# Performance work log

Measured on AMD Instinct MI355X. Metric: run time of the kernel, lower is better.

Reference implementation:

```python
import jax, jax.numpy as jnp
import numpy as np

T, B, C = 2048, 8, 1024
HEAD_SIZE = 128
HEAD_OUT = 128


def setup_inputs() -> dict:
    key = jax.random.key(0)
    kq, kk, kv, kwq, kwk, kwv = jax.random.split(key, 6)
    q = jax.random.normal(kq, (T, B, C), dtype=jnp.float32)
    k = jax.random.normal(kk, (T, B, C), dtype=jnp.float32)
    v = jax.random.normal(kv, (T, B, C), dtype=jnp.float32)
    # additive causal mask: 0 on/below diagonal, -1e9 above
    mask = jnp.where(jnp.tril(jnp.ones((T, T), dtype=bool)), 0.0, -1e9).astype(jnp.float32)
    # linear weights stored as [in, out] (torch Linear weight is [out,in], applied as x @ W.T)
    s = 1.0 / np.sqrt(C)
    Wq = jax.random.uniform(kwq, (C, HEAD_SIZE), minval=-s, maxval=s, dtype=jnp.float32)
    Wk = jax.random.uniform(kwk, (C, HEAD_SIZE), minval=-s, maxval=s, dtype=jnp.float32)
    Wv = jax.random.uniform(kwv, (C, HEAD_OUT), minval=-s, maxval=s, dtype=jnp.float32)
    return {"q": q, "k": k, "v": v, "mask": mask, "Wq": Wq, "Wk": Wk, "Wv": Wv}


def reference(q, k, v, mask, Wq, Wk, Wv):
    # q,k,v: [T,B,C] (time-major, as in the torch module)
    Q = jnp.einsum('tbc,ch->tbh', q, Wq)           # [T,B,H]
    K = jnp.einsum('tbc,ch->tbh', k, Wk)           # [T,B,H]
    V = jnp.einsum('tbc,co->tbo', v, Wv)           # [T,B,O]
    scale = HEAD_SIZE ** -0.5
    scores = jnp.einsum('tbh,sbh->bts', Q, K) * scale  # [B,T,T]
    scores = scores + mask[None, :, :]
    weights = jax.nn.softmax(scores, axis=-1)          # [B,T,T]
    ctx = jnp.einsum('bts,sbo->tbo', weights, V)       # [T,B,O]
    return ctx
```

## Files before the change

kernel.cpp:

```cpp
#include <hip/hip_runtime.h>

typedef _Float16 f16_t;
typedef _Float16 f16x4 __attribute__((ext_vector_type(4)));
typedef _Float16 f16x8 __attribute__((ext_vector_type(8)));
typedef float f32x4 __attribute__((ext_vector_type(4)));

#define T_DIM 2048
#define B_DIM 8
#define C_DIM 1024
#define H_DIM 128

__device__ __forceinline__ void gload16(const void* g, void* l) {
  __builtin_amdgcn_global_load_lds((const __attribute__((address_space(1))) void*)g,
                                   (__attribute__((address_space(3))) void*)l, 16, 0, 0);
}

__global__ __launch_bounds__(256) void wprep_kernel(
    const float* __restrict__ Wq, const float* __restrict__ Wk, const float* __restrict__ Wv,
    f16_t* __restrict__ Wtq, f16_t* __restrict__ Wtk, f16_t* __restrict__ Wtv) {
  int z = blockIdx.x;
  const float* src = (z == 0) ? Wq : (z == 1) ? Wk : Wv;
  f16_t* dst = (z == 0) ? Wtq : (z == 1) ? Wtk : Wtv;
  float sc = (z == 0) ? (1.4426950408889634f * 0.08838834764831845f) : 1.0f;
  int base = blockIdx.y * 2048;
  for (int i = threadIdx.x; i < 2048; i += 256) {
    int idx = base + i;
    int c = idx >> 7, h = idx & 127;
    dst[h * C_DIM + c] = (f16_t)(src[idx] * sc);
  }
}

__global__ __launch_bounds__(256) void proj_kernel(
    const float* __restrict__ qin, const float* __restrict__ kin, const float* __restrict__ vin,
    const f16_t* __restrict__ Wtq, const f16_t* __restrict__ Wtk, const f16_t* __restrict__ Wtv,
    f16_t* __restrict__ Qh, f16_t* __restrict__ Kh, f16_t* __restrict__ Vt) {
  int z = blockIdx.y;
  const float* src = (z == 0) ? qin : (z == 1) ? kin : vin;
  const f16_t* Wt = (z == 0) ? Wtq : (z == 1) ? Wtk : Wtv;

  __shared__ f16_t Alds[64][72];
  __shared__ f16_t Wlds[128][72];

  int tid = threadIdx.x;
  int wid = tid >> 6, lane = tid & 63, g = lane >> 4, lr = lane & 15;
  int wr = (wid >> 1) * 32, wc = (wid & 1) * 64;
  int rbase = blockIdx.x * 64;

  const f32x4 z4 = {0.0f, 0.0f, 0.0f, 0.0f};
  f32x4 acc[2][4];
#pragma unroll
  for (int i = 0; i < 2; ++i)
#pragma unroll
    for (int j = 0; j < 4; ++j) acc[i][j] = z4;

  for (int kb = 0; kb < C_DIM; kb += 64) {
    __syncthreads();
#pragma unroll
    for (int p = 0; p < 4; ++p) {
      int row = p * 16 + (tid >> 4);
      int col = (tid & 15) * 4;
      const float* gp = src + (size_t)(rbase + row) * C_DIM + kb + col;
      f32x4 a4 = *(const f32x4*)gp;
      f16x4 h4;
      h4[0] = (f16_t)a4[0]; h4[1] = (f16_t)a4[1]; h4[2] = (f16_t)a4[2]; h4[3] = (f16_t)a4[3];
      *(f16x4*)&Alds[row][col] = h4;
    }
#pragma unroll
    for (int p = 0; p < 4; ++p) {
      int row = p * 32 + (tid >> 3);
      int col = (tid & 7) * 8;
      *(f16x8*)&Wlds[row][col] = *(const f16x8*)(Wt + row * C_DIM + kb + col);
    }
    __syncthreads();
#pragma unroll
    for (int c = 0; c < 2; ++c) {
      f16x8 af[2], bfr[4];
#pragma unroll
      for (int rf = 0; rf < 2; ++rf) af[rf] = *(const f16x8*)&Alds[wr + rf * 16 + lr][c * 32 + g * 8];
#pragma unroll
      for (int cf = 0; cf < 4; ++cf) bfr[cf] = *(const f16x8*)&Wlds[wc + cf * 16 + lr][c * 32 + g * 8];
#pragma unroll
      for (int rf = 0; rf < 2; ++rf)
#pragma unroll
        for (int cf = 0; cf < 4; ++cf)
          acc[rf][cf] = __builtin_amdgcn_mfma_f32_16x16x32_f16(af[rf], bfr[cf], acc[rf][cf], 0, 0, 0);
    }
  }

  if (z < 2) {
    f16_t* outp = (z == 0) ? Qh : Kh;
#pragma unroll
    for (int rf = 0; rf < 2; ++rf)
#pragma unroll
      for (int cf = 0; cf < 4; ++cf)
#pragma unroll
        for (int r = 0; r < 4; ++r) {
          int rg = rbase + wr + rf * 16 + g * 4 + r;
          int t = rg >> 3, bb = rg & 7;
          int h = wc + cf * 16 + lr;
          outp[(size_t)((bb << 11) | t) * H_DIM + h] = (f16_t)acc[rf][cf][r];
        }
  } else {
#pragma unroll
    for (int rf = 0; rf < 2; ++rf)
#pragma unroll
      for (int cf = 0; cf < 4; ++cf)
#pragma unroll
        for (int r = 0; r < 4; ++r) {
          int rg = rbase + wr + rf * 16 + g * 4 + r;
          int t = rg >> 3, bb = rg & 7;
          int h = wc + cf * 16 + lr;
          Vt[((size_t)bb << 18) | ((size_t)h << 11) | (size_t)t] = (f16_t)acc[rf][cf][r];
        }
  }
}

__global__ __launch_bounds__(256) void attn_kernel(
    const f16_t* __restrict__ Qh, const f16_t* __restrict__ Kh, const f16_t* __restrict__ Vt,
    float* __restrict__ out) {
  int b = blockIdx.x;
  int qt = (gridDim.y - 1) - blockIdx.y;
  int tid = threadIdx.x;
  int wid = tid >> 6, lane = tid & 63, g = lane >> 4, lr = lane & 15;
  int qlo = qt * 64 + wid * 16;

  __shared__ f16_t Kl[64 * 128];
  __shared__ f16_t Vl[2][128 * 64];
  __shared__ f16_t Plds[4][16][72];

  const f16_t* Qb = Qh + ((size_t)b << 11) * H_DIM;
  const f16_t* Kb = Kh + ((size_t)b << 11) * H_DIM;
  const f16_t* Vb = Vt + ((size_t)b << 18);

  f16x8 qa[4];
#pragma unroll
  for (int c = 0; c < 4; ++c)
    qa[c] = *(const f16x8*)&Qb[(size_t)(qlo + lr) * H_DIM + c * 32 + g * 8];

  const f32x4 z4 = {0.0f, 0.0f, 0.0f, 0.0f};
  float mrow[4], lsum[4];
  f32x4 acc[8];
#pragma unroll
  for (int r = 0; r < 4; ++r) { mrow[r] = -1e30f; lsum[r] = 0.0f; }
#pragma unroll
  for (int of = 0; of < 8; ++of) acc[of] = z4;

  int ntiles = qt + 1;

  auto stageK = [&](int kt) {
    const char* base = (const char*)(Kb + (size_t)(kt * 64) * H_DIM);
#pragma unroll
    for (int i = 0; i < 4; ++i) {
      int chunk = wid * 4 + i;
      int q = chunk * 1024 + lane * 16;
      int p = q ^ (((q >> 8) & 7) << 4);
      gload16(base + p, (char*)&Kl[0] + q);
    }
  };
  auto stageV = [&](int bufi, int kt) {
#pragma unroll
    for (int i = 0; i < 4; ++i) {
      int chunk = wid * 4 + i;
      int q = chunk * 1024 + lane * 16;
      int p = q ^ (((q >> 7) & 7) << 4);
      int row = p >> 7;
      int colb = p & 127;
      const char* src = (const char*)(Vb + (size_t)row * T_DIM + kt * 64) + colb;
      gload16(src, (char*)&Vl[bufi][0] + q);
    }
  };

  stageK(0);
  stageV(0, 0);
  __syncthreads();
  int vcur = 0;

  for (int kt = 0; kt < ntiles; ++kt) {
    int kb = kt * 64;
    bool more = (kt + 1 < ntiles);
    if (more) stageV(vcur ^ 1, kt + 1);

    f32x4 s[4];
#pragma unroll
    for (int cf = 0; cf < 4; ++cf) s[cf] = z4;
    const char* Kbuf = (const char*)&Kl[0];
#pragma unroll
    for (int cf = 0; cf < 4; ++cf) {
      int row = cf * 16 + lr;
#pragma unroll
      for (int c = 0; c < 4; ++c) {
        int linb = row * 256 + c * 64 + g * 16;
        f16x8 kf = *(const f16x8*)(Kbuf + (linb ^ ((row & 7) << 4)));
        s[cf] = __builtin_amdgcn_mfma_f32_16x16x32_f16(qa[c], kf, s[cf], 0, 0, 0);
      }
    }
    __syncthreads();
    if (more) stageK(kt + 1);

    if (kb + 63 > qlo) {
#pragma unroll
      for (int cf = 0; cf < 4; ++cf) {
        int kcol = kb + cf * 16 + lr;
#pragma unroll
        for (int r = 0; r < 4; ++r)
          if (kcol > qlo + g * 4 + r) s[cf][r] = -1e30f;
      }
    }
    float cand[4], mnew[4], al[4], rs[4];
#pragma unroll
    for (int r = 0; r < 4; ++r)
      cand[r] = fmaxf(fmaxf(s[0][r], s[1][r]), fmaxf(s[2][r], s[3][r]));
#pragma unroll
    for (int d = 1; d <= 8; d <<= 1)
#pragma unroll
      for (int r = 0; r < 4; ++r)
        cand[r] = fmaxf(cand[r], __shfl_xor(cand[r], d));
    float p[4][4];
#pragma unroll
    for (int r = 0; r < 4; ++r) {
      mnew[r] = fmaxf(mrow[r], cand[r]);
      al[r] = exp2f(mrow[r] - mnew[r]);
      mrow[r] = mnew[r];
    }
#pragma unroll
    for (int cf = 0; cf < 4; ++cf)
#pragma unroll
      for (int r = 0; r < 4; ++r)
        p[cf][r] = exp2f(s[cf][r] - mnew[r]);
#pragma unroll
    for (int r = 0; r < 4; ++r)
      rs[r] = (p[0][r] + p[1][r]) + (p[2][r] + p[3][r]);
#pragma unroll
    for (int d = 1; d <= 8; d <<= 1)
#pragma unroll
      for (int r = 0; r < 4; ++r)
        rs[r] += __shfl_xor(rs[r], d);
#pragma unroll
    for (int r = 0; r < 4; ++r)
      lsum[r] = lsum[r] * al[r] + rs[r];
#pragma unroll
    for (int of = 0; of < 8; ++of)
#pragma unroll
      for (int r = 0; r < 4; ++r)
        acc[of][r] *= al[r];
#pragma unroll
    for (int cf = 0; cf < 4; ++cf)
#pragma unroll
      for (int r = 0; r < 4; ++r)
        Plds[wid][g * 4 + r][cf * 16 + lr] = (f16_t)p[cf][r];
    asm volatile("s_waitcnt lgkmcnt(0)" ::: "memory");
    __builtin_amdgcn_sched_barrier(0);
    f16x8 pa[2];
#pragma unroll
    for (int c = 0; c < 2; ++c)
      pa[c] = *(const f16x8*)&Plds[wid][lr][c * 32 + g * 8];

    const char* Vbuf = (const char*)&Vl[vcur][0];
#pragma unroll
    for (int c = 0; c < 2; ++c)
#pragma unroll
      for (int of = 0; of < 8; ++of) {
        int row = of * 16 + lr;
        int linb = row * 128 + c * 64 + g * 16;
        f16x8 vf = *(const f16x8*)(Vbuf + (linb ^ ((row & 7) << 4)));
        acc[of] = __builtin_amdgcn_mfma_f32_16x16x32_f16(pa[c], vf, acc[of], 0, 0, 0);
      }
    __syncthreads();
    vcur ^= 1;
  }

#pragma unroll
  for (int of = 0; of < 8; ++of)
#pragma unroll
    for (int r = 0; r < 4; ++r) {
      int qr = qlo + g * 4 + r;
      out[(size_t)(qr * 8 + b) * H_DIM + of * 16 + lr] = acc[of][r] / lsum[r];
    }
}

extern "C" void kernel_launch(void* const* d_in, const int* in_sizes, int n_in,
                              void* d_out, int out_size, void* d_ws, size_t ws_size,
                              hipStream_t stream) {
  const float* q = (const float*)d_in[0];
  const float* k = (const float*)d_in[1];
  const float* v = (const float*)d_in[2];
  const float* Wq = (const float*)d_in[4];
  const float* Wk = (const float*)d_in[5];
  const float* Wv = (const float*)d_in[6];
  float* out = (float*)d_out;

  char* ws = (char*)d_ws;
  f16_t* Qh = (f16_t*)(ws);
  f16_t* Kh = (f16_t*)(ws + (4u << 20));
  f16_t* Vt = (f16_t*)(ws + (8u << 20));
  f16_t* Wtq = (f16_t*)(ws + (12u << 20));
  f16_t* Wtk = (f16_t*)(ws + (12u << 20) + (256u << 10));
  f16_t* Wtv = (f16_t*)(ws + (12u << 20) + (512u << 10));

  hipLaunchKernelGGL(wprep_kernel, dim3(3, 64), dim3(256), 0, stream, Wq, Wk, Wv, Wtq, Wtk, Wtv);
  hipLaunchKernelGGL(proj_kernel, dim3(256, 3), dim3(256), 0, stream, q, k, v, Wtq, Wtk, Wtv, Qh, Kh, Vt);
  hipLaunchKernelGGL(attn_kernel, dim3(8, 32), dim3(256), 0, stream, Qh, Kh, Vt, out);
}
```

Baseline: 121.9 us.

## Double-buffer projection GEMM with async global-to-LDS loads and XOR swizzle

Rewrites the projection kernel's k-loop to stage the fp32 activation tile and fp16 weight tile directly into LDS with global_load_lds into two buffers, prefetching the next tile while MFMAs run on the current one. The fp32-to-fp16 conversion moves from the staging step to the fragment read. An XOR swizzle replaces the old row padding to avoid bank conflicts. LDS use grows (fp32 A tile, two buffers), which may reduce occupancy, and there is no explicit wait on the async loads before the barrier beyond what __syncthreads implies.

```diff
diff --git a/kernel.cpp b/kernel.cpp
--- a/kernel.cpp
+++ b/kernel.cpp
@@ -38,8 +38,8 @@
   const float* src = (z == 0) ? qin : (z == 1) ? kin : vin;
   const f16_t* Wt = (z == 0) ? Wtq : (z == 1) ? Wtk : Wtv;
 
-  __shared__ f16_t Alds[64][72];
-  __shared__ f16_t Wlds[128][72];
+  __shared__ float Al[2][64 * 64];
+  __shared__ f16_t Wl[2][128 * 64];
 
   int tid = threadIdx.x;
   int wid = tid >> 6, lane = tid & 63, g = lane >> 4, lr = lane & 15;
@@ -53,38 +53,70 @@
 #pragma unroll
     for (int j = 0; j < 4; ++j) acc[i][j] = z4;
 
-  for (int kb = 0; kb < C_DIM; kb += 64) {
-    __syncthreads();
-#pragma unroll
-    for (int p = 0; p < 4; ++p) {
-      int row = p * 16 + (tid >> 4);
-      int col = (tid & 15) * 4;
-      const float* gp = src + (size_t)(rbase + row) * C_DIM + kb + col;
-      f32x4 a4 = *(const f32x4*)gp;
-      f16x4 h4;
-      h4[0] = (f16_t)a4[0]; h4[1] = (f16_t)a4[1]; h4[2] = (f16_t)a4[2]; h4[3] = (f16_t)a4[3];
-      *(f16x4*)&Alds[row][col] = h4;
-    }
-#pragma unroll
-    for (int p = 0; p < 4; ++p) {
-      int row = p * 32 + (tid >> 3);
-      int col = (tid & 7) * 8;
-      *(f16x8*)&Wlds[row][col] = *(const f16x8*)(Wt + row * C_DIM + kb + col);
-    }
-    __syncthreads();
-#pragma unroll
-    for (int c = 0; c < 2; ++c) {
+  auto stageA = [&](int bufi, int kb) {
+    const char* base = (const char*)(src + (size_t)rbase * C_DIM + kb);
+    char* ldsb = (char*)&Al[bufi][0];
+#pragma unroll
+    for (int i = 0; i < 4; ++i) {
+      int q = (wid * 4 + i) * 1024 + lane * 16;
+      int p = q ^ (((q >> 8) & 7) << 4);
+      int row = p >> 8, colb = p & 255;
+      gload16(base + (size_t)row * 4096 + colb, ldsb + q);
+    }
+  };
+  auto stageW = [&](int bufi, int kb) {
+    const char* base = (const char*)(Wt + kb);
+    char* ldsb = (char*)&Wl[bufi][0];
+#pragma unroll
+    for (int i = 0; i < 4; ++i) {
+      int q = (wid * 4 + i) * 1024 + lane * 16;
+      int p = q ^ (((q >> 7) & 7) << 4);
+      int row = p >> 7, colb = p & 127;
+      gload16(base + (size_t)row * 2048 + colb, ldsb + q);
+    }
+  };
+
+  stageA(0, 0);
+  stageW(0, 0);
+  __syncthreads();
+
+  int buf = 0;
+  for (int kt = 0; kt < 16; ++kt) {
+    if (kt + 1 < 16) {
+      stageA(buf ^ 1, (kt + 1) * 64);
+      stageW(buf ^ 1, (kt + 1) * 64);
+    }
+    const char* Ab = (const char*)&Al[buf][0];
+    const char* Wb = (const char*)&Wl[buf][0];
+#pragma unroll
+    for (int k2 = 0; k2 < 2; ++k2) {
       f16x8 af[2], bfr[4];
 #pragma unroll
-      for (int rf = 0; rf < 2; ++rf) af[rf] = *(const f16x8*)&Alds[wr + rf * 16 + lr][c * 32 + g * 8];
-#pragma unroll
-      for (int cf = 0; cf < 4; ++cf) bfr[cf] = *(const f16x8*)&Wlds[wc + cf * 16 + lr][c * 32 + g * 8];
+      for (int rf = 0; rf < 2; ++rf) {
+        int row = wr + rf * 16 + lr;
+        int sw = (row & 7) << 4;
+        int b0 = row * 256 + k2 * 128 + g * 32;
+        f32x4 lo = *(const f32x4*)(Ab + (b0 ^ sw));
+        f32x4 hi = *(const f32x4*)(Ab + ((b0 + 16) ^ sw));
+        f16x8 h;
+        h[0] = (f16_t)lo[0]; h[1] = (f16_t)lo[1]; h[2] = (f16_t)lo[2]; h[3] = (f16_t)lo[3];
+        h[4] = (f16_t)hi[0]; h[5] = (f16_t)hi[1]; h[6] = (f16_t)hi[2]; h[7] = (f16_t)hi[3];
+        af[rf] = h;
+      }
+#pragma unroll
+      for (int cf = 0; cf < 4; ++cf) {
+        int row = wc + cf * 16 + lr;
+        int b0 = (row * 128 + k2 * 64 + g * 16) ^ ((row & 7) << 4);
+        bfr[cf] = *(const f16x8*)(Wb + b0);
+      }
 #pragma unroll
       for (int rf = 0; rf < 2; ++rf)
 #pragma unroll
         for (int cf = 0; cf < 4; ++cf)
           acc[rf][cf] = __builtin_amdgcn_mfma_f32_16x16x32_f16(af[rf], bfr[cf], acc[rf][cf], 0, 0, 0);
     }
+    __syncthreads();
+    buf ^= 1;
   }
 
   if (z < 2) {
```

Result: slower. 144.9 us (+18.9%).

## Rewrite projection as single-wave LDS-free MFMA kernel loading fragments directly

Applied to the files above, without the earlier changes.

The projection kernel now runs one 64-lane wave per block, each computing a 32x128 tile. It loads A and W fragments straight from global memory into registers and converts them to f16, with no shared-memory staging and no barriers. The grid doubles to 512 row tiles per input. This removes LDS round-trips and syncs, but each wave now reads the full 128-column weight slice on its own with strided, uncoalesced 16-byte loads that rely on cache reuse. Register pressure also rises with 16 accumulators.

```diff
diff --git a/kernel.cpp b/kernel.cpp
--- a/kernel.cpp
+++ b/kernel.cpp
@@ -30,7 +30,7 @@
   }
 }
 
-__global__ __launch_bounds__(256) void proj_kernel(
+__global__ __launch_bounds__(64, 2) void proj_kernel(
     const float* __restrict__ qin, const float* __restrict__ kin, const float* __restrict__ vin,
     const f16_t* __restrict__ Wtq, const f16_t* __restrict__ Wtk, const f16_t* __restrict__ Wtv,
     f16_t* __restrict__ Qh, f16_t* __restrict__ Kh, f16_t* __restrict__ Vt) {
@@ -38,52 +38,41 @@
   const float* src = (z == 0) ? qin : (z == 1) ? kin : vin;
   const f16_t* Wt = (z == 0) ? Wtq : (z == 1) ? Wtk : Wtv;
 
-  __shared__ f16_t Alds[64][72];
-  __shared__ f16_t Wlds[128][72];
-
-  int tid = threadIdx.x;
-  int wid = tid >> 6, lane = tid & 63, g = lane >> 4, lr = lane & 15;
-  int wr = (wid >> 1) * 32, wc = (wid & 1) * 64;
-  int rbase = blockIdx.x * 64;
+  int lane = threadIdx.x;
+  int g = lane >> 4, lr = lane & 15;
+  int rbase = blockIdx.x * 32;
+
+  const float* a0 = src + (size_t)(rbase + lr) * C_DIM + g * 8;
+  const float* a1 = src + (size_t)(rbase + 16 + lr) * C_DIM + g * 8;
+  const f16_t* wb = Wt + (size_t)lr * C_DIM + g * 8;
 
   const f32x4 z4 = {0.0f, 0.0f, 0.0f, 0.0f};
-  f32x4 acc[2][4];
+  f32x4 acc[2][8];
 #pragma unroll
   for (int i = 0; i < 2; ++i)
 #pragma unroll
-    for (int j = 0; j < 4; ++j) acc[i][j] = z4;
-
-  for (int kb = 0; kb < C_DIM; kb += 64) {
-    __syncthreads();
-#pragma unroll
-    for (int p = 0; p < 4; ++p) {
-      int row = p * 16 + (tid >> 4);
-      int col = (tid & 15) * 4;
-      const float* gp = src + (size_t)(rbase + row) * C_DIM + kb + col;
-      f32x4 a4 = *(const f32x4*)gp;
-      f16x4 h4;
-      h4[0] = (f16_t)a4[0]; h4[1] = (f16_t)a4[1]; h4[2] = (f16_t)a4[2]; h4[3] = (f16_t)a4[3];
-      *(f16x4*)&Alds[row][col] = h4;
-    }
-#pragma unroll
-    for (int p = 0; p < 4; ++p) {
-      int row = p * 32 + (tid >> 3);
-      int col = (tid & 7) * 8;
-      *(f16x8*)&Wlds[row][col] = *(const f16x8*)(Wt + row * C_DIM + kb + col);
-    }
-    __syncthreads();
-#pragma unroll
-    for (int c = 0; c < 2; ++c) {
-      f16x8 af[2], bfr[4];
-#pragma unroll
-      for (int rf = 0; rf < 2; ++rf) af[rf] = *(const f16x8*)&Alds[wr + rf * 16 + lr][c * 32 + g * 8];
-#pragma unroll
-      for (int cf = 0; cf < 4; ++cf) bfr[cf] = *(const f16x8*)&Wlds[wc + cf * 16 + lr][c * 32 + g * 8];
-#pragma unroll
-      for (int rf = 0; rf < 2; ++rf)
-#pragma unroll
-        for (int cf = 0; cf < 4; ++cf)
-          acc[rf][cf] = __builtin_amdgcn_mfma_f32_16x16x32_f16(af[rf], bfr[cf], acc[rf][cf], 0, 0, 0);
+    for (int j = 0; j < 8; ++j) acc[i][j] = z4;
+
+#pragma unroll 4
+  for (int kt = 0; kt < 32; ++kt) {
+    int ko = kt * 32;
+    f32x4 l0 = *(const f32x4*)(a0 + ko);
+    f32x4 h0 = *(const f32x4*)(a0 + ko + 4);
+    f32x4 l1 = *(const f32x4*)(a1 + ko);
+    f32x4 h1 = *(const f32x4*)(a1 + ko + 4);
+    f16x8 wf[8];
+#pragma unroll
+    for (int cf = 0; cf < 8; ++cf)
+      wf[cf] = *(const f16x8*)(wb + (size_t)cf * 16 * C_DIM + ko);
+    f16x8 af0, af1;
+    af0[0] = (f16_t)l0[0]; af0[1] = (f16_t)l0[1]; af0[2] = (f16_t)l0[2]; af0[3] = (f16_t)l0[3];
+    af0[4] = (f16_t)h0[0]; af0[5] = (f16_t)h0[1]; af0[6] = (f16_t)h0[2]; af0[7] = (f16_t)h0[3];
+    af1[0] = (f16_t)l1[0]; af1[1] = (f16_t)l1[1]; af1[2] = (f16_t)l1[2]; af1[3] = (f16_t)l1[3];
+    af1[4] = (f16_t)h1[0]; af1[5] = (f16_t)h1[1]; af1[6] = (f16_t)h1[2]; af1[7] = (f16_t)h1[3];
+#pragma unroll
+    for (int cf = 0; cf < 8; ++cf) {
+      acc[0][cf] = __builtin_amdgcn_mfma_f32_16x16x32_f16(af0, wf[cf], acc[0][cf], 0, 0, 0);
+      acc[1][cf] = __builtin_amdgcn_mfma_f32_16x16x32_f16(af1, wf[cf], acc[1][cf], 0, 0, 0);
     }
   }
 
@@ -92,24 +81,24 @@
 #pragma unroll
     for (int rf = 0; rf < 2; ++rf)
 #pragma unroll
-      for (int cf = 0; cf < 4; ++cf)
+      for (int cf = 0; cf < 8; ++cf)
 #pragma unroll
         for (int r = 0; r < 4; ++r) {
-          int rg = rbase + wr + rf * 16 + g * 4 + r;
+          int rg = rbase + rf * 16 + g * 4 + r;
           int t = rg >> 3, bb = rg & 7;
-          int h = wc + cf * 16 + lr;
+          int h = cf * 16 + lr;
           outp[(size_t)((bb << 11) | t) * H_DIM + h] = (f16_t)acc[rf][cf][r];
         }
   } else {
 #pragma unroll
     for (int rf = 0; rf < 2; ++rf)
 #pragma unroll
-      for (int cf = 0; cf < 4; ++cf)
+      for (int cf = 0; cf < 8; ++cf)
 #pragma unroll
         for (int r = 0; r < 4; ++r) {
-          int rg = rbase + wr + rf * 16 + g * 4 + r;
+          int rg = rbase + rf * 16 + g * 4 + r;
           int t = rg >> 3, bb = rg & 7;
-          int h = wc + cf * 16 + lr;
+          int h = cf * 16 + lr;
           Vt[((size_t)bb << 18) | ((size_t)h << 11) | (size_t)t] = (f16_t)acc[rf][cf][r];
         }
   }
@@ -298,6 +287,6 @@
   f16_t* Wtv = (f16_t*)(ws + (12u << 20) + (512u << 10));
 
   hipLaunchKernelGGL(wprep_kernel, dim3(3, 64), dim3(256), 0, stream, Wq, Wk, Wv, Wtq, Wtk, Wtv);
-  hipLaunchKernelGGL(proj_kernel, dim3(256, 3), dim3(256), 0, stream, q, k, v, Wtq, Wtk, Wtv, Qh, Kh, Vt);
+  hipLaunchKernelGGL(proj_kernel, dim3(512, 3), dim3(64), 0, stream, q, k, v, Wtq, Wtk, Wtv, Qh, Kh, Vt);
   hipLaunchKernelGGL(attn_kernel, dim3(8, 32), dim3(256), 0, stream, Qh, Kh, Vt, out);
 }
```

New measurement: 176.4 us. +44.6%, slower.

## Restructure projection: stage full-K A rows in LDS, stream weights from global

Applied to the files above, without the earlier changes.

The projection kernel now loads a 32-row by 1024-column fp32 input tile once, converts it to fp16 into LDS, and drops the per-k-step double-sync loop. Each wave computes a 16x64 output tile, reading weight fragments straight from global/L2 with a one-step register prefetch. The grid doubles to 512 blocks per projection and launch bounds request 2 blocks per CU. This removes the repeated barriers and the LDS staging of weights, with the aim of better latency hiding on the memory-bound input read. In exchange, weight reads from L2 go up, and the roughly 66KB LDS per block may limit occupancy.

```diff
diff --git a/kernel.cpp b/kernel.cpp
--- a/kernel.cpp
+++ b/kernel.cpp
@@ -9,6 +9,9 @@
 #define B_DIM 8
 #define C_DIM 1024
 #define H_DIM 128
+
+#define AROWS 32
+#define ASTRIDE 1032
 
 __device__ __forceinline__ void gload16(const void* g, void* l) {
   __builtin_amdgcn_global_load_lds((const __attribute__((address_space(1))) void*)g,
@@ -30,7 +33,7 @@
   }
 }
 
-__global__ __launch_bounds__(256) void proj_kernel(
+__global__ __launch_bounds__(256, 2) void proj_kernel(
     const float* __restrict__ qin, const float* __restrict__ kin, const float* __restrict__ vin,
     const f16_t* __restrict__ Wtq, const f16_t* __restrict__ Wtk, const f16_t* __restrict__ Wtv,
     f16_t* __restrict__ Qh, f16_t* __restrict__ Kh, f16_t* __restrict__ Vt) {
@@ -38,80 +41,88 @@
   const float* src = (z == 0) ? qin : (z == 1) ? kin : vin;
   const f16_t* Wt = (z == 0) ? Wtq : (z == 1) ? Wtk : Wtv;
 
-  __shared__ f16_t Alds[64][72];
-  __shared__ f16_t Wlds[128][72];
+  __shared__ f16_t Al[AROWS * ASTRIDE];
 
   int tid = threadIdx.x;
   int wid = tid >> 6, lane = tid & 63, g = lane >> 4, lr = lane & 15;
-  int wr = (wid >> 1) * 32, wc = (wid & 1) * 64;
-  int rbase = blockIdx.x * 64;
-
+  int rbase = blockIdx.x * AROWS;
+
+#pragma unroll
+  for (int half = 0; half < 2; ++half) {
+    f32x4 v[16];
+#pragma unroll
+    for (int rr = 0; rr < 4; ++rr) {
+      const float* rowp = src + (size_t)(rbase + wid * 8 + half * 4 + rr) * C_DIM;
+#pragma unroll
+      for (int j = 0; j < 4; ++j)
+        v[rr * 4 + j] = *(const f32x4*)(rowp + j * 256 + lane * 4);
+    }
+#pragma unroll
+    for (int rr = 0; rr < 4; ++rr) {
+      int r = wid * 8 + half * 4 + rr;
+#pragma unroll
+      for (int j = 0; j < 4; ++j) {
+        f32x4 a = v[rr * 4 + j];
+        f16x4 h;
+        h[0] = (f16_t)a[0]; h[1] = (f16_t)a[1]; h[2] = (f16_t)a[2]; h[3] = (f16_t)a[3];
+        *(f16x4*)&Al[r * ASTRIDE + j * 256 + lane * 4] = h;
+      }
+    }
+  }
+  __syncthreads();
+
+  int wr = (wid & 1) * 16, wc = (wid >> 1) * 64;
   const f32x4 z4 = {0.0f, 0.0f, 0.0f, 0.0f};
-  f32x4 acc[2][4];
-#pragma unroll
-  for (int i = 0; i < 2; ++i)
-#pragma unroll
-    for (int j = 0; j < 4; ++j) acc[i][j] = z4;
-
-  for (int kb = 0; kb < C_DIM; kb += 64) {
-    __syncthreads();
-#pragma unroll
-    for (int p = 0; p < 4; ++p) {
-      int row = p * 16 + (tid >> 4);
-      int col = (tid & 15) * 4;
-      const float* gp = src + (size_t)(rbase + row) * C_DIM + kb + col;
-      f32x4 a4 = *(const f32x4*)gp;
-      f16x4 h4;
-      h4[0] = (f16_t)a4[0]; h4[1] = (f16_t)a4[1]; h4[2] = (f16_t)a4[2]; h4[3] = (f16_t)a4[3];
-      *(f16x4*)&Alds[row][col] = h4;
-    }
-#pragma unroll
-    for (int p = 0; p < 4; ++p) {
-      int row = p * 32 + (tid >> 3);
-      int col = (tid & 7) * 8;
-      *(f16x8*)&Wlds[row][col] = *(const f16x8*)(Wt + row * C_DIM + kb + col);
-    }
-    __syncthreads();
-#pragma unroll
-    for (int c = 0; c < 2; ++c) {
-      f16x8 af[2], bfr[4];
-#pragma unroll
-      for (int rf = 0; rf < 2; ++rf) af[rf] = *(const f16x8*)&Alds[wr + rf * 16 + lr][c * 32 + g * 8];
-#pragma unroll
-      for (int cf = 0; cf < 4; ++cf) bfr[cf] = *(const f16x8*)&Wlds[wc + cf * 16 + lr][c * 32 + g * 8];
-#pragma unroll
-      for (int rf = 0; rf < 2; ++rf)
-#pragma unroll
-        for (int cf = 0; cf < 4; ++cf)
-          acc[rf][cf] = __builtin_amdgcn_mfma_f32_16x16x32_f16(af[rf], bfr[cf], acc[rf][cf], 0, 0, 0);
-    }
+  f32x4 acc[4];
+#pragma unroll
+  for (int j = 0; j < 4; ++j) acc[j] = z4;
+
+  const f16_t* wb = Wt + (size_t)(wc + lr) * C_DIM + g * 8;
+  const f16_t* arow = &Al[(wr + lr) * ASTRIDE + g * 8];
+
+  f16x8 wfn[4];
+#pragma unroll
+  for (int cf = 0; cf < 4; ++cf)
+    wfn[cf] = *(const f16x8*)(wb + (size_t)cf * 16 * C_DIM);
+
+#pragma unroll 2
+  for (int kt = 0; kt < 32; ++kt) {
+    f16x8 wf[4];
+#pragma unroll
+    for (int cf = 0; cf < 4; ++cf) wf[cf] = wfn[cf];
+    if (kt < 31) {
+      int ko = (kt + 1) * 32;
+#pragma unroll
+      for (int cf = 0; cf < 4; ++cf)
+        wfn[cf] = *(const f16x8*)(wb + (size_t)cf * 16 * C_DIM + ko);
+    }
+    f16x8 af = *(const f16x8*)(arow + kt * 32);
+#pragma unroll
+    for (int cf = 0; cf < 4; ++cf)
+      acc[cf] = __builtin_amdgcn_mfma_f32_16x16x32_f16(af, wf[cf], acc[cf], 0, 0, 0);
   }
 
   if (z < 2) {
     f16_t* outp = (z == 0) ? Qh : Kh;
 #pragma unroll
-    for (int rf = 0; rf < 2; ++rf)
-#pragma unroll
-      for (int cf = 0; cf < 4; ++cf)
-#pragma unroll
-        for (int r = 0; r < 4; ++r) {
-          int rg = rbase + wr + rf * 16 + g * 4 + r;
-          int t = rg >> 3, bb = rg & 7;
-          int h = wc + cf * 16 + lr;
-          outp[(size_t)((bb << 11) | t) * H_DIM + h] = (f16_t)acc[rf][cf][r];
-        }
+    for (int cf = 0; cf < 4; ++cf)
+#pragma unroll
+      for (int r = 0; r < 4; ++r) {
+        int rg = rbase + wr + g * 4 + r;
+        int t = rg >> 3, bb = rg & 7;
+        int h = wc + cf * 16 + lr;
+        outp[(size_t)((bb << 11) | t) * H_DIM + h] = (f16_t)acc[cf][r];
+      }
   } else {
 #pragma unroll
-    for (int rf = 0; rf < 2; ++rf)
-#pragma unroll
-      for (int cf = 0; cf < 4; ++cf)
-#pragma unroll
-        for (int r = 0; r < 4; ++r) {
-          int rg = rbase + wr + rf * 16 + g * 4 + r;
-          int t = rg >> 3, bb = rg & 7;
-          int h = wc + cf * 16 + lr;
-          Vt[((size_t)bb << 18) | ((size_t)h << 11) | (size_t)t] = (f16_t)acc[rf][cf][r];
-        }
+    for (int cf = 0; cf < 4; ++cf)
+#pragma unroll
+      for (int r = 0; r < 4; ++r) {
+        int rg = rbase + wr + g * 4 + r;
+        int t = rg >> 3, bb = rg & 7;
+        int h = wc + cf * 16 + lr;
+        Vt[((size_t)bb << 18) | ((size_t)h << 11) | (size_t)t] = (f16_t)acc[cf][r];
+      }
   }
 }
 
@@ -298,6 +309,6 @@
   f16_t* Wtv = (f16_t*)(ws + (12u << 20) + (512u << 10));
 
   hipLaunchKernelGGL(wprep_kernel, dim3(3, 64), dim3(256), 0, stream, Wq, Wk, Wv, Wtq, Wtk, Wtv);
-  hipLaunchKernelGGL(proj_kernel, dim3(256, 3), dim3(256), 0, stream, q, k, v, Wtq, Wtk, Wtv, Qh, Kh, Vt);
+  hipLaunchKernelGGL(proj_kernel, dim3(512, 3), dim3(256), 0, stream, q, k, v, Wtq, Wtk, Wtv, Qh, Kh, Vt);
   hipLaunchKernelGGL(attn_kernel, dim3(8, 32), dim3(256), 0, stream, Qh, Kh, Vt, out);
 }
```

Result: slower. 197.8 us (+62.2%).
